# Kernel optimization log

Measured on AMD Instinct MI355X. Metric: run time of the kernel, lower is better.

Reference implementation:

```python
import jax, jax.numpy as jnp
import numpy as np

NUM_ITERATIONS = 3


def _squash_elementwise(s):
    # Faithful to original: squared_norm summed over trailing axis of size 1
    # => elementwise squash v = s^2 * s / ((1 + s^2) * sqrt(s^2))
    sq = s * s
    return sq * s / ((1.0 + sq) * jnp.sqrt(sq))


def setup_inputs() -> dict:
    key = jax.random.key(0)
    k1, k2 = jax.random.split(key)
    B, R, C, O, I = 256, 1152, 10, 16, 8
    x = jax.random.normal(k1, (B, R, I), dtype=jnp.float32)
    W = jax.random.normal(k2, (R, C, O, I), dtype=jnp.float32)
    return {"x": x, "W": W}


def reference(x, W):
    # x: (B, R, I); W: (R, C, O, I)
    R, C, O, I = W.shape
    # u_hat[b,r,c,o] = sum_i W[r,c,o,i] * x[b,r,i]   (matmul W @ x per route/capsule)
    u_hat = jnp.einsum('rcoi,bri->brco', W, x)  # (B, R, C, O)
    b_ij = jnp.zeros((R, C), dtype=x.dtype)  # batch-shared routing logits
    v = None
    for it in range(NUM_ITERATIONS):
        c_ij = jax.nn.softmax(b_ij, axis=0)  # softmax over routes (dim=1 in torch)
        s_j = jnp.einsum('rc,brco->bco', c_ij, u_hat)  # weighted sum over routes
        v = _squash_elementwise(s_j)  # (B, C, O)
        if it < NUM_ITERATIONS - 1:
            # agreement a[b,r,c] = u_hat[b,r,c,:] . v[b,c,:]
            a_ij = jnp.einsum('brco,bco->brc', u_hat, v)
            b_ij = b_ij + a_ij.mean(axis=0)  # mean over batch, batch-shared update
    return v[..., None]  # (B, C, O, 1) matches v_j.squeeze(1)
```

## Files before the change

### kernel.cpp

```cpp
#include <hip/hip_runtime.h>

static constexpr int B_ = 256;
static constexpr int R_ = 1152;
static constexpr int C_ = 10;
static constexpr int O_ = 16;
static constexpr int I_ = 8;
static constexpr int SCO = C_ * O_;
static constexpr int K_ = R_ * I_;
static constexpr int NB = 256;

typedef short bf16x8 __attribute__((ext_vector_type(8)));
typedef float f32x4  __attribute__((ext_vector_type(4)));

__device__ __forceinline__ unsigned short f2bf(float f) {
  union { float f; unsigned int u; } c; c.f = f;
  const unsigned int u = c.u;
  return (unsigned short)((u + 0x7fffu + ((u >> 16) & 1u)) >> 16);
}
__device__ __forceinline__ float bf2f(unsigned short h) {
  union { unsigned int u; float f; } c; c.u = ((unsigned int)h) << 16; return c.f;
}

__device__ __forceinline__ void gsync(unsigned int* bar, unsigned int epoch) {
  __syncthreads();
  if (threadIdx.x == 0)
    __hip_atomic_store(&bar[blockIdx.x * 16], epoch,
                       __ATOMIC_RELEASE, __HIP_MEMORY_SCOPE_AGENT);
  if (blockIdx.x == 0) {
    if (threadIdx.x < 256) {
      int guard = 0;
      while (__hip_atomic_load(&bar[threadIdx.x * 16],
                               __ATOMIC_RELAXED, __HIP_MEMORY_SCOPE_AGENT) < epoch) {
        __builtin_amdgcn_s_sleep(8);
        if (++guard > (1 << 17)) break;
      }
    }
    __syncthreads();
    if (threadIdx.x < 8)
      __hip_atomic_store(&bar[4096 + threadIdx.x * 16], epoch,
                         __ATOMIC_RELEASE, __HIP_MEMORY_SCOPE_AGENT);
  } else {
    if (threadIdx.x == 0) {
      unsigned int* g = &bar[4096 + (blockIdx.x & 7) * 16];
      int guard = 0;
      while (__hip_atomic_load(g, __ATOMIC_RELAXED,
                               __HIP_MEMORY_SCOPE_AGENT) < epoch) {
        __builtin_amdgcn_s_sleep(32);
        if (++guard > (1 << 16)) break;
      }
    }
  }
  __syncthreads();
  asm volatile("" ::: "memory");
}

__global__ __launch_bounds__(512, 1) void mega(
    const float* __restrict__ x, const float* __restrict__ W,
    float* __restrict__ out, unsigned int* __restrict__ bar,
    float* __restrict__ bvec, float* __restrict__ Z,
    unsigned short* __restrict__ xb, unsigned short* __restrict__ wraw,
    unsigned short* __restrict__ xT,
    unsigned short* __restrict__ vb0, unsigned short* __restrict__ vb1,
    unsigned short* __restrict__ wb2a, unsigned short* __restrict__ wb2b) {
  __shared__ __align__(16) unsigned char smem[82560];
  const int bx = blockIdx.x;
  const int t = threadIdx.x;
  const int lane = t & 63;
  const int w = __builtin_amdgcn_readfirstlane(t >> 6);
  const int mrow = lane & 15, quad = lane >> 4;

  if (bx == 0 && t < 32) Z[t] = 0.0f;

  if (bx < 160) {
    float* sred = (float*)smem;
    const int g = (bx & 7) * 20 + (bx >> 3);
    const int mtile = g / 10, c = g - mtile * 10;
    const int m0 = mtile * 16;
    const float* apf = x + (size_t)(m0 + mrow) * K_ + w * 1152 + quad * 8;
    const float* bpf = W + ((size_t)(w * 144 + quad) * C_ + c) * 128 + mrow * 8;
    f32x4 acc = {0.0f, 0.0f, 0.0f, 0.0f};
#pragma unroll 4
    for (int kk = 0; kk < 36; ++kk) {
      const float4 a0 = *(const float4*)(apf + kk * 32);
      const float4 a1 = *(const float4*)(apf + kk * 32 + 4);
      const float4 b0 = *(const float4*)(bpf + (size_t)kk * 5120);
      const float4 b1 = *(const float4*)(bpf + (size_t)kk * 5120 + 4);
      bf16x8 a, b;
      a[0] = (short)f2bf(a0.x); a[1] = (short)f2bf(a0.y);
      a[2] = (short)f2bf(a0.z); a[3] = (short)f2bf(a0.w);
      a[4] = (short)f2bf(a1.x); a[5] = (short)f2bf(a1.y);
      a[6] = (short)f2bf(a1.z); a[7] = (short)f2bf(a1.w);
      b[0] = (short)f2bf(b0.x); b[1] = (short)f2bf(b0.y);
      b[2] = (short)f2bf(b0.z); b[3] = (short)f2bf(b0.w);
      b[4] = (short)f2bf(b1.x); b[5] = (short)f2bf(b1.y);
      b[6] = (short)f2bf(b1.z); b[7] = (short)f2bf(b1.w);
      acc = __builtin_amdgcn_mfma_f32_16x16x32_bf16(a, b, acc, 0, 0, 0);
    }
#pragma unroll
    for (int rg = 0; rg < 4; ++rg)
      sred[w * 272 + mrow * 17 + quad * 4 + rg] = acc[rg];
    __syncthreads();
    if (t < 256) {
      const int n = t >> 4, m = t & 15;
      const int e = n * 17 + m;
      const float ss = ((sred[0 * 272 + e] + sred[1 * 272 + e]) +
                        (sred[2 * 272 + e] + sred[3 * 272 + e])) +
                       ((sred[4 * 272 + e] + sred[5 * 272 + e]) +
                        (sred[6 * 272 + e] + sred[7 * 272 + e]));
      const float s = ss * (1.0f / 1152.0f);
      const float v = s * fabsf(s) / (1.0f + s * s);
      vb0[(size_t)(c * 16 + n) * 256 + m0 + m] = f2bf(v);
    }
  } else {
    const float4* wf = (const float4*)W;
    ushort4* wr = (ushort4*)wraw;
    for (int idx = t; idx < 3840; idx += 512) {
      const int j = (bx - 160) * 3840 + idx;
      const float4 v4 = wf[j];
      ushort4 r4;
      r4.x = f2bf(v4.x); r4.y = f2bf(v4.y); r4.z = f2bf(v4.z); r4.w = f2bf(v4.w);
      wr[j] = r4;
    }
    float* sx = (float*)smem;
    for (int u = bx - 160; u < 256; u += 96) {
      const int bq = u & 3, rseg = u >> 2;
      const int rbase = rseg * 18;
      __syncthreads();
      for (int idx = t; idx < 64 * 36; idx += 512) {
        const int b = idx / 36, f4 = idx - b * 36;
        const size_t off = (size_t)(bq * 64 + b) * K_ + rbase * I_ + f4 * 4;
        const float4 val = *(const float4*)(x + off);
        ushort4 o4;
        o4.x = f2bf(val.x); o4.y = f2bf(val.y); o4.z = f2bf(val.z); o4.w = f2bf(val.w);
        *(ushort4*)(xb + off) = o4;
        const int rr = f4 >> 1, i4 = (f4 & 1) * 4;
        sx[(rr * 8 + i4 + 0) * 68 + b] = val.x;
        sx[(rr * 8 + i4 + 1) * 68 + b] = val.y;
        sx[(rr * 8 + i4 + 2) * 68 + b] = val.z;
        sx[(rr * 8 + i4 + 3) * 68 + b] = val.w;
      }
      __syncthreads();
      for (int row = w * 18; row < w * 18 + 18; ++row)
        xT[(size_t)(rseg * 144 + row) * 256 + bq * 64 + lane] = f2bf(sx[row * 68 + lane]);
    }
  }
  gsync(bar, 1);

  for (int it = 0; it < 2; ++it) {
    if (bx < 72) {
      unsigned short* svb = (unsigned short*)smem;
      float* sp = (float*)smem;
      float* sbs = (float*)(smem + 81920);
      const unsigned short* vbr = (it == 0) ? vb0 : vb1;
      unsigned short* wb2w = (it == 0) ? wb2a : wb2b;
      const int seg = (bx & 7) * 9 + (bx >> 3);
      const int r0 = seg * 16;
      const unsigned short* ap = xT + (size_t)(seg * 128 + w * 16 + mrow) * 256 + quad * 8;
      bf16x8 afr[8];
#pragma unroll
      for (int kk = 0; kk < 8; ++kk) afr[kk] = *(const bf16x8*)(ap + kk * 32);
      {
        const char* src = (const char*)vbr;
        char* dst = (char*)svb;
#pragma unroll
        for (int i = 0; i < 10; ++i) {
          const int ci = i * 512 + t;
          const int lin = ci * 16;
          const int n = ci >> 5;
          *(bf16x8*)(dst + (lin ^ ((n & 7) << 4))) = *(const bf16x8*)(src + lin);
        }
      }
      __syncthreads();
      f32x4 acc[10];
#pragma unroll
      for (int c = 0; c < 10; ++c) acc[c] = (f32x4){0.0f, 0.0f, 0.0f, 0.0f};
#pragma unroll
      for (int c = 0; c < 10; ++c) {
        const int n = c * 16 + mrow;
        const int base = n * 512 + quad * 16;
#pragma unroll
        for (int kk = 0; kk < 8; ++kk) {
          const bf16x8 b = *(const bf16x8*)((const char*)svb +
                            ((base + kk * 64) ^ ((n & 7) << 4)));
          acc[c] = __builtin_amdgcn_mfma_f32_16x16x32_bf16(afr[kk], b, acc[c], 0, 0, 0);
        }
      }
      __syncthreads();
#pragma unroll
      for (int c = 0; c < 10; ++c)
#pragma unroll
        for (int rg = 0; rg < 4; ++rg) {
          const int ml = w * 16 + quad * 4 + rg;
          sp[(c * 16 + (ml >> 3)) * 128 + mrow * 8 + (ml & 7)] = acc[c][rg];
        }
      __syncthreads();
      const int p16 = t >> 5, l32 = t & 31;
#pragma unroll
      for (int ch = 0; ch < 10; ++ch) {
        const int pair = ch * 16 + p16;
        const int rl = pair / 10, c = pair - rl * 10;
        const float4 pv = *(const float4*)&sp[(c * 16 + rl) * 128 + l32 * 4];
        const float4 wv = *(const float4*)(W + (size_t)(r0 + rl) * 1280 + c * 128 + l32 * 4);
        float prod = wv.x * pv.x + wv.y * pv.y + wv.z * pv.z + wv.w * pv.w;
        prod += __shfl_xor(prod, 1);  prod += __shfl_xor(prod, 2);
        prod += __shfl_xor(prod, 4);  prod += __shfl_xor(prod, 8);
        prod += __shfl_xor(prod, 16);
        if (l32 == 0) sbs[rl * 10 + c] = prod;
      }
      __syncthreads();
      if (t < 160) {
        const int rl = t / 10, c = t - rl * 10;
        const int r = r0 + rl;
        float b = sbs[t] * (1.0f / 256.0f);
        if (it != 0) b += bvec[r * C_ + c];
        bvec[r * C_ + c] = b;
        sbs[t] = expf(b);
      }
      __syncthreads();
      if (t < 10) {
        float z = 0.0f;
#pragma unroll
        for (int rl = 0; rl < 16; ++rl) z += sbs[rl * 10 + t];
        atomicAdd(&Z[(it + 1) * 10 + t], z);
      }
#pragma unroll
      for (int i = 0; i < 5; ++i) {
        const int base = i * 4096 + t * 8;
        const int rl = base / 1280, rem2 = base - rl * 1280;
        const int c = rem2 >> 7;
        const float e = sbs[rl * 10 + c];
        const size_t off = ((size_t)(r0 + rl) * C_ + c) * 128 + (rem2 & 127);
        const bf16x8 wv8 = *(const bf16x8*)(wraw + off);
        bf16x8 o8;
#pragma unroll
        for (int j = 0; j < 8; ++j)
          o8[j] = (short)f2bf(bf2f((unsigned short)wv8[j]) * e);
        *(bf16x8*)(wb2w + off) = o8;
      }
    }
    gsync(bar, 2 + 2 * it);

    {
      const int git = it + 1;
      if (bx < 160) {
        float* sred = (float*)smem;
        float* szed = (float*)(smem + 16384);
        const unsigned short* Bm = (git == 1) ? wb2a : wb2b;
        const int g = (bx & 7) * 20 + (bx >> 3);
        const int mtile = g / 10, c = g - mtile * 10;
        const int m0 = mtile * 16;
        const unsigned short* ap = xb + (size_t)(m0 + mrow) * K_ + w * 1152 + quad * 8;
        const unsigned short* bp = Bm + ((size_t)(w * 144 + quad) * C_ + c) * 128 + mrow * 8;
        if (t < 10) szed[t] = atomicAdd(&Z[git * 10 + t], 0.0f);
        f32x4 acc = {0.0f, 0.0f, 0.0f, 0.0f};
#pragma unroll 6
        for (int kk = 0; kk < 36; ++kk) {
          const bf16x8 a = *(const bf16x8*)(ap + kk * 32);
          const bf16x8 b = *(const bf16x8*)(bp + (size_t)kk * 5120);
          acc = __builtin_amdgcn_mfma_f32_16x16x32_bf16(a, b, acc, 0, 0, 0);
        }
#pragma unroll
        for (int rg = 0; rg < 4; ++rg)
          sred[w * 272 + mrow * 17 + quad * 4 + rg] = acc[rg];
        __syncthreads();
        if (t < 256) {
          int m, n;
          if (git == 2) { m = t >> 4; n = t & 15; } else { n = t >> 4; m = t & 15; }
          const int e = n * 17 + m;
          const float ss = ((sred[0 * 272 + e] + sred[1 * 272 + e]) +
                            (sred[2 * 272 + e] + sred[3 * 272 + e])) +
                           ((sred[4 * 272 + e] + sred[5 * 272 + e]) +
                            (sred[6 * 272 + e] + sred[7 * 272 + e]));
          const float s = ss / szed[c];
          const float v = s * fabsf(s) / (1.0f + s * s);
          if (git == 2) out[(size_t)(m0 + m) * SCO + c * 16 + n] = v;
          else          vb1[(size_t)(c * 16 + n) * 256 + m0 + m] = f2bf(v);
        }
      }
    }
    if (it == 0) gsync(bar, 3);
  }
}

extern "C" void kernel_launch(void* const* d_in, const int* in_sizes, int n_in,
                              void* d_out, int out_size, void* d_ws, size_t ws_size,
                              hipStream_t stream) {
  const float* x = (const float*)d_in[0];
  const float* W = (const float*)d_in[1];
  float* out = (float*)d_out;

  unsigned int* bar = (unsigned int*)d_ws;
  float* bvec = (float*)d_ws + 4224;
  float* Z    = bvec + R_ * C_;
  unsigned short* xb   = (unsigned short*)(Z + 32);
  unsigned short* wraw = xb + (size_t)B_ * K_;
  unsigned short* xT   = wraw + (size_t)R_ * C_ * O_ * I_;
  unsigned short* vb0  = xT + (size_t)R_ * 8 * 256;
  unsigned short* vb1  = vb0 + (size_t)160 * 256;
  unsigned short* wb2a = vb1 + (size_t)160 * 256;
  unsigned short* wb2b = wb2a + (size_t)R_ * C_ * O_ * I_;

  hipMemsetAsync(bar, 0, 16896, stream);
  mega<<<NB, 512, 0, stream>>>(x, W, out, bar, bvec, Z, xb, wraw, xT,
                               vb0, vb1, wb2a, wb2b);
}
```

Baseline: 161.5 us.

## Fold routing softmax weights into GEMM B-load instead of materializing scaled W

Removes the pre-scaled bf16 weight buffers (wb2a/wb2b). Each GEMM phase now loads the raw bf16 W and multiplies it by exp(b) weights held in LDS just before the MFMA. The preprocessing is spread evenly across all 256 blocks, so the first GEMM reads bf16 data instead of converting fp32 on the fly at the cost of one more grid barrier. The agreement phase is also split across 144 blocks of 8 routes each, with only 4 waves doing MFMA. This saves a full write and re-read of the scaled W per iteration, but adds conversion ALU work inside the GEMM inner loop.

Result: faster. 150.5 us (-6.8%).

```diff
diff --git a/kernel.cpp b/kernel.cpp
--- a/kernel.cpp
+++ b/kernel.cpp
@@ -54,14 +54,163 @@
   asm volatile("" ::: "memory");
 }
 
+__device__ __forceinline__ void gemm_phase(
+    int git, const unsigned short* __restrict__ xb,
+    const unsigned short* __restrict__ wraw, const float* __restrict__ eX,
+    float* __restrict__ Z, unsigned short* __restrict__ vbw,
+    float* __restrict__ out, unsigned char* smem,
+    int bx, int t, int w, int mrow, int quad) {
+  float* sred = (float*)smem;
+  float* szed = (float*)(smem + 16384);
+  float* e_lds = (float*)(smem + 20480);
+  const int xcd = bx & 7, j = bx >> 3;
+  const int mtile = (xcd >> 1) * 4 + j / 5;
+  const int c = (xcd & 1) * 5 + j % 5;
+  const int m0 = mtile * 16;
+  if (git > 0) {
+    for (int idx = t; idx < 1152; idx += 512) e_lds[idx] = eX[c * 1152 + idx];
+    if (t < 10) szed[t] = atomicAdd(&Z[git * 10 + t], 0.0f);
+    __syncthreads();
+  }
+  const unsigned short* ap = xb + (size_t)(m0 + mrow) * K_ + w * 1152 + quad * 8;
+  const unsigned short* bp = wraw + ((size_t)(w * 144 + quad) * C_ + c) * 128 + mrow * 8;
+  f32x4 acc = {0.0f, 0.0f, 0.0f, 0.0f};
+  if (git == 0) {
+#pragma unroll 6
+    for (int kk = 0; kk < 36; ++kk) {
+      const bf16x8 a = *(const bf16x8*)(ap + kk * 32);
+      const bf16x8 b = *(const bf16x8*)(bp + (size_t)kk * 5120);
+      acc = __builtin_amdgcn_mfma_f32_16x16x32_bf16(a, b, acc, 0, 0, 0);
+    }
+  } else {
+#pragma unroll 6
+    for (int kk = 0; kk < 36; ++kk) {
+      const bf16x8 a = *(const bf16x8*)(ap + kk * 32);
+      const bf16x8 braw = *(const bf16x8*)(bp + (size_t)kk * 5120);
+      const float ev = e_lds[w * 144 + kk * 4 + quad];
+      bf16x8 b;
+#pragma unroll
+      for (int j8 = 0; j8 < 8; ++j8)
+        b[j8] = (short)f2bf(bf2f((unsigned short)braw[j8]) * ev);
+      acc = __builtin_amdgcn_mfma_f32_16x16x32_bf16(a, b, acc, 0, 0, 0);
+    }
+  }
+#pragma unroll
+  for (int rg = 0; rg < 4; ++rg)
+    sred[w * 272 + mrow * 17 + quad * 4 + rg] = acc[rg];
+  __syncthreads();
+  if (t < 256) {
+    int m, n;
+    if (git == 2) { m = t >> 4; n = t & 15; } else { n = t >> 4; m = t & 15; }
+    const int e = n * 17 + m;
+    const float ss = ((sred[0 * 272 + e] + sred[1 * 272 + e]) +
+                      (sred[2 * 272 + e] + sred[3 * 272 + e])) +
+                     ((sred[4 * 272 + e] + sred[5 * 272 + e]) +
+                      (sred[6 * 272 + e] + sred[7 * 272 + e]));
+    const float s = (git == 0) ? ss * (1.0f / 1152.0f) : ss / szed[c];
+    const float v = s * fabsf(s) / (1.0f + s * s);
+    if (git == 2) out[(size_t)(m0 + m) * SCO + c * 16 + n] = v;
+    else          vbw[(size_t)(c * 16 + n) * 256 + m0 + m] = f2bf(v);
+  }
+}
+
+__device__ __forceinline__ void pv_phase(
+    int it, const unsigned short* __restrict__ xT,
+    const unsigned short* __restrict__ vbr, const float* __restrict__ W,
+    const unsigned short* __restrict__ wraw_unused,
+    float* __restrict__ bvec, float* __restrict__ eOut, float* __restrict__ Z,
+    unsigned char* smem, int bx, int t, int lane, int w, int mrow, int quad) {
+  unsigned short* svb = (unsigned short*)smem;
+  float* sp = (float*)smem;
+  float* sbs = (float*)(smem + 81920);
+  const int seg = (bx & 7) * 18 + (bx >> 3);
+  const int r0 = seg * 8;
+  bf16x8 afr[8];
+  if (w < 4) {
+    const unsigned short* ap = xT + (size_t)(seg * 64 + w * 16 + mrow) * 256 + quad * 8;
+#pragma unroll
+    for (int kk = 0; kk < 8; ++kk) afr[kk] = *(const bf16x8*)(ap + kk * 32);
+  }
+  {
+    const char* src = (const char*)vbr;
+    char* dst = (char*)svb;
+#pragma unroll
+    for (int i = 0; i < 10; ++i) {
+      const int ci = i * 512 + t;
+      const int lin = ci * 16;
+      const int n = ci >> 5;
+      *(bf16x8*)(dst + (lin ^ ((n & 7) << 4))) = *(const bf16x8*)(src + lin);
+    }
+  }
+  __syncthreads();
+  f32x4 acc[10];
+  if (w < 4) {
+#pragma unroll
+    for (int c = 0; c < 10; ++c) acc[c] = (f32x4){0.0f, 0.0f, 0.0f, 0.0f};
+#pragma unroll
+    for (int c = 0; c < 10; ++c) {
+      const int n = c * 16 + mrow;
+      const int base = n * 512 + quad * 16;
+#pragma unroll
+      for (int kk = 0; kk < 8; ++kk) {
+        const bf16x8 b = *(const bf16x8*)((const char*)svb +
+                          ((base + kk * 64) ^ ((n & 7) << 4)));
+        acc[c] = __builtin_amdgcn_mfma_f32_16x16x32_bf16(afr[kk], b, acc[c], 0, 0, 0);
+      }
+    }
+  }
+  __syncthreads();
+  if (w < 4) {
+#pragma unroll
+    for (int c = 0; c < 10; ++c)
+#pragma unroll
+      for (int rg = 0; rg < 4; ++rg) {
+        const int ml = w * 16 + quad * 4 + rg;
+        sp[(c * 8 + (ml >> 3)) * 128 + mrow * 8 + (ml & 7)] = acc[c][rg];
+      }
+  }
+  __syncthreads();
+  const int p16 = t >> 5, l32 = t & 31;
+#pragma unroll
+  for (int ch = 0; ch < 5; ++ch) {
+    const int pair = ch * 16 + p16;
+    const int rl = pair / 10, c = pair - rl * 10;
+    const float4 pv4 = *(const float4*)&sp[(c * 8 + rl) * 128 + l32 * 4];
+    const float4 wv = *(const float4*)(W + (size_t)(r0 + rl) * 1280 + c * 128 + l32 * 4);
+    float prod = wv.x * pv4.x + wv.y * pv4.y + wv.z * pv4.z + wv.w * pv4.w;
+    prod += __shfl_xor(prod, 1);  prod += __shfl_xor(prod, 2);
+    prod += __shfl_xor(prod, 4);  prod += __shfl_xor(prod, 8);
+    prod += __shfl_xor(prod, 16);
+    if (l32 == 0) sbs[rl * 10 + c] = prod;
+  }
+  __syncthreads();
+  if (t < 80) {
+    const int rl = t / 10, c = t - rl * 10;
+    const int r = r0 + rl;
+    float b = sbs[t] * (1.0f / 256.0f);
+    if (it != 0) b += bvec[r * C_ + c];
+    bvec[r * C_ + c] = b;
+    const float e = expf(b);
+    sbs[t] = e;
+    eOut[c * 1152 + r] = e;
+  }
+  __syncthreads();
+  if (t < 10) {
+    float z = 0.0f;
+#pragma unroll
+    for (int rl = 0; rl < 8; ++rl) z += sbs[rl * 10 + t];
+    atomicAdd(&Z[(it + 1) * 10 + t], z);
+  }
+}
+
 __global__ __launch_bounds__(512, 1) void mega(
     const float* __restrict__ x, const float* __restrict__ W,
     float* __restrict__ out, unsigned int* __restrict__ bar,
     float* __restrict__ bvec, float* __restrict__ Z,
+    float* __restrict__ eA, float* __restrict__ eB,
     unsigned short* __restrict__ xb, unsigned short* __restrict__ wraw,
     unsigned short* __restrict__ xT,
-    unsigned short* __restrict__ vb0, unsigned short* __restrict__ vb1,
-    unsigned short* __restrict__ wb2a, unsigned short* __restrict__ wb2b) {
+    unsigned short* __restrict__ vb0, unsigned short* __restrict__ vb1) {
   __shared__ __align__(16) unsigned char smem[82560];
   const int bx = blockIdx.x;
   const int t = threadIdx.x;
@@ -69,217 +218,52 @@
   const int w = __builtin_amdgcn_readfirstlane(t >> 6);
   const int mrow = lane & 15, quad = lane >> 4;
 
-  if (bx == 0 && t < 32) Z[t] = 0.0f;
-
-  if (bx < 160) {
-    float* sred = (float*)smem;
-    const int g = (bx & 7) * 20 + (bx >> 3);
-    const int mtile = g / 10, c = g - mtile * 10;
-    const int m0 = mtile * 16;
-    const float* apf = x + (size_t)(m0 + mrow) * K_ + w * 1152 + quad * 8;
-    const float* bpf = W + ((size_t)(w * 144 + quad) * C_ + c) * 128 + mrow * 8;
-    f32x4 acc = {0.0f, 0.0f, 0.0f, 0.0f};
-#pragma unroll 4
-    for (int kk = 0; kk < 36; ++kk) {
-      const float4 a0 = *(const float4*)(apf + kk * 32);
-      const float4 a1 = *(const float4*)(apf + kk * 32 + 4);
-      const float4 b0 = *(const float4*)(bpf + (size_t)kk * 5120);
-      const float4 b1 = *(const float4*)(bpf + (size_t)kk * 5120 + 4);
-      bf16x8 a, b;
-      a[0] = (short)f2bf(a0.x); a[1] = (short)f2bf(a0.y);
-      a[2] = (short)f2bf(a0.z); a[3] = (short)f2bf(a0.w);
-      a[4] = (short)f2bf(a1.x); a[5] = (short)f2bf(a1.y);
-      a[6] = (short)f2bf(a1.z); a[7] = (short)f2bf(a1.w);
-      b[0] = (short)f2bf(b0.x); b[1] = (short)f2bf(b0.y);
-      b[2] = (short)f2bf(b0.z); b[3] = (short)f2bf(b0.w);
-      b[4] = (short)f2bf(b1.x); b[5] = (short)f2bf(b1.y);
-      b[6] = (short)f2bf(b1.z); b[7] = (short)f2bf(b1.w);
-      acc = __builtin_amdgcn_mfma_f32_16x16x32_bf16(a, b, acc, 0, 0, 0);
-    }
-#pragma unroll
-    for (int rg = 0; rg < 4; ++rg)
-      sred[w * 272 + mrow * 17 + quad * 4 + rg] = acc[rg];
-    __syncthreads();
-    if (t < 256) {
-      const int n = t >> 4, m = t & 15;
-      const int e = n * 17 + m;
-      const float ss = ((sred[0 * 272 + e] + sred[1 * 272 + e]) +
-                        (sred[2 * 272 + e] + sred[3 * 272 + e])) +
-                       ((sred[4 * 272 + e] + sred[5 * 272 + e]) +
-                        (sred[6 * 272 + e] + sred[7 * 272 + e]));
-      const float s = ss * (1.0f / 1152.0f);
-      const float v = s * fabsf(s) / (1.0f + s * s);
-      vb0[(size_t)(c * 16 + n) * 256 + m0 + m] = f2bf(v);
-    }
-  } else {
+  {
     const float4* wf = (const float4*)W;
     ushort4* wr = (ushort4*)wraw;
-    for (int idx = t; idx < 3840; idx += 512) {
-      const int j = (bx - 160) * 3840 + idx;
+    for (int idx = t; idx < 1440; idx += 512) {
+      const int j = bx * 1440 + idx;
       const float4 v4 = wf[j];
       ushort4 r4;
       r4.x = f2bf(v4.x); r4.y = f2bf(v4.y); r4.z = f2bf(v4.z); r4.w = f2bf(v4.w);
       wr[j] = r4;
     }
+    if (bx == 0 && t < 32) Z[t] = 0.0f;
     float* sx = (float*)smem;
-    for (int u = bx - 160; u < 256; u += 96) {
-      const int bq = u & 3, rseg = u >> 2;
-      const int rbase = rseg * 18;
-      __syncthreads();
-      for (int idx = t; idx < 64 * 36; idx += 512) {
-        const int b = idx / 36, f4 = idx - b * 36;
-        const size_t off = (size_t)(bq * 64 + b) * K_ + rbase * I_ + f4 * 4;
-        const float4 val = *(const float4*)(x + off);
-        ushort4 o4;
-        o4.x = f2bf(val.x); o4.y = f2bf(val.y); o4.z = f2bf(val.z); o4.w = f2bf(val.w);
-        *(ushort4*)(xb + off) = o4;
-        const int rr = f4 >> 1, i4 = (f4 & 1) * 4;
-        sx[(rr * 8 + i4 + 0) * 68 + b] = val.x;
-        sx[(rr * 8 + i4 + 1) * 68 + b] = val.y;
-        sx[(rr * 8 + i4 + 2) * 68 + b] = val.z;
-        sx[(rr * 8 + i4 + 3) * 68 + b] = val.w;
-      }
-      __syncthreads();
-      for (int row = w * 18; row < w * 18 + 18; ++row)
-        xT[(size_t)(rseg * 144 + row) * 256 + bq * 64 + lane] = f2bf(sx[row * 68 + lane]);
-    }
+    const int bq = bx & 3, rseg = bx >> 2;
+    const int rbase = rseg * 18;
+    for (int idx = t; idx < 64 * 36; idx += 512) {
+      const int b = idx / 36, f4 = idx - b * 36;
+      const size_t off = (size_t)(bq * 64 + b) * K_ + rbase * I_ + f4 * 4;
+      const float4 val = *(const float4*)(x + off);
+      ushort4 o4;
+      o4.x = f2bf(val.x); o4.y = f2bf(val.y); o4.z = f2bf(val.z); o4.w = f2bf(val.w);
+      *(ushort4*)(xb + off) = o4;
+      const int rr = f4 >> 1, i4 = (f4 & 1) * 4;
+      sx[(rr * 8 + i4 + 0) * 68 + b] = val.x;
+      sx[(rr * 8 + i4 + 1) * 68 + b] = val.y;
+      sx[(rr * 8 + i4 + 2) * 68 + b] = val.z;
+      sx[(rr * 8 + i4 + 3) * 68 + b] = val.w;
+    }
+    __syncthreads();
+    for (int row = w * 18; row < w * 18 + 18; ++row)
+      xT[(size_t)(rseg * 144 + row) * 256 + bq * 64 + lane] = f2bf(sx[row * 68 + lane]);
   }
   gsync(bar, 1);
 
-  for (int it = 0; it < 2; ++it) {
-    if (bx < 72) {
-      unsigned short* svb = (unsigned short*)smem;
-      float* sp = (float*)smem;
-      float* sbs = (float*)(smem + 81920);
-      const unsigned short* vbr = (it == 0) ? vb0 : vb1;
-      unsigned short* wb2w = (it == 0) ? wb2a : wb2b;
-      const int seg = (bx & 7) * 9 + (bx >> 3);
-      const int r0 = seg * 16;
-      const unsigned short* ap = xT + (size_t)(seg * 128 + w * 16 + mrow) * 256 + quad * 8;
-      bf16x8 afr[8];
-#pragma unroll
-      for (int kk = 0; kk < 8; ++kk) afr[kk] = *(const bf16x8*)(ap + kk * 32);
-      {
-        const char* src = (const char*)vbr;
-        char* dst = (char*)svb;
-#pragma unroll
-        for (int i = 0; i < 10; ++i) {
-          const int ci = i * 512 + t;
-          const int lin = ci * 16;
-          const int n = ci >> 5;
-          *(bf16x8*)(dst + (lin ^ ((n & 7) << 4))) = *(const bf16x8*)(src + lin);
-        }
-      }
-      __syncthreads();
-      f32x4 acc[10];
-#pragma unroll
-      for (int c = 0; c < 10; ++c) acc[c] = (f32x4){0.0f, 0.0f, 0.0f, 0.0f};
-#pragma unroll
-      for (int c = 0; c < 10; ++c) {
-        const int n = c * 16 + mrow;
-        const int base = n * 512 + quad * 16;
-#pragma unroll
-        for (int kk = 0; kk < 8; ++kk) {
-          const bf16x8 b = *(const bf16x8*)((const char*)svb +
-                            ((base + kk * 64) ^ ((n & 7) << 4)));
-          acc[c] = __builtin_amdgcn_mfma_f32_16x16x32_bf16(afr[kk], b, acc[c], 0, 0, 0);
-        }
-      }
-      __syncthreads();
-#pragma unroll
-      for (int c = 0; c < 10; ++c)
-#pragma unroll
-        for (int rg = 0; rg < 4; ++rg) {
-          const int ml = w * 16 + quad * 4 + rg;
-          sp[(c * 16 + (ml >> 3)) * 128 + mrow * 8 + (ml & 7)] = acc[c][rg];
-        }
-      __syncthreads();
-      const int p16 = t >> 5, l32 = t & 31;
-#pragma unroll
-      for (int ch = 0; ch < 10; ++ch) {
-        const int pair = ch * 16 + p16;
-        const int rl = pair / 10, c = pair - rl * 10;
-        const float4 pv = *(const float4*)&sp[(c * 16 + rl) * 128 + l32 * 4];
-        const float4 wv = *(const float4*)(W + (size_t)(r0 + rl) * 1280 + c * 128 + l32 * 4);
-        float prod = wv.x * pv.x + wv.y * pv.y + wv.z * pv.z + wv.w * pv.w;
-        prod += __shfl_xor(prod, 1);  prod += __shfl_xor(prod, 2);
-        prod += __shfl_xor(prod, 4);  prod += __shfl_xor(prod, 8);
-        prod += __shfl_xor(prod, 16);
-        if (l32 == 0) sbs[rl * 10 + c] = prod;
-      }
-      __syncthreads();
-      if (t < 160) {
-        const int rl = t / 10, c = t - rl * 10;
-        const int r = r0 + rl;
-        float b = sbs[t] * (1.0f / 256.0f);
-        if (it != 0) b += bvec[r * C_ + c];
-        bvec[r * C_ + c] = b;
-        sbs[t] = expf(b);
-      }
-      __syncthreads();
-      if (t < 10) {
-        float z = 0.0f;
-#pragma unroll
-        for (int rl = 0; rl < 16; ++rl) z += sbs[rl * 10 + t];
-        atomicAdd(&Z[(it + 1) * 10 + t], z);
-      }
-#pragma unroll
-      for (int i = 0; i < 5; ++i) {
-        const int base = i * 4096 + t * 8;
-        const int rl = base / 1280, rem2 = base - rl * 1280;
-        const int c = rem2 >> 7;
-        const float e = sbs[rl * 10 + c];
-        const size_t off = ((size_t)(r0 + rl) * C_ + c) * 128 + (rem2 & 127);
-        const bf16x8 wv8 = *(const bf16x8*)(wraw + off);
-        bf16x8 o8;
-#pragma unroll
-        for (int j = 0; j < 8; ++j)
-          o8[j] = (short)f2bf(bf2f((unsigned short)wv8[j]) * e);
-        *(bf16x8*)(wb2w + off) = o8;
-      }
-    }
-    gsync(bar, 2 + 2 * it);
-
-    {
-      const int git = it + 1;
-      if (bx < 160) {
-        float* sred = (float*)smem;
-        float* szed = (float*)(smem + 16384);
-        const unsigned short* Bm = (git == 1) ? wb2a : wb2b;
-        const int g = (bx & 7) * 20 + (bx >> 3);
-        const int mtile = g / 10, c = g - mtile * 10;
-        const int m0 = mtile * 16;
-        const unsigned short* ap = xb + (size_t)(m0 + mrow) * K_ + w * 1152 + quad * 8;
-        const unsigned short* bp = Bm + ((size_t)(w * 144 + quad) * C_ + c) * 128 + mrow * 8;
-        if (t < 10) szed[t] = atomicAdd(&Z[git * 10 + t], 0.0f);
-        f32x4 acc = {0.0f, 0.0f, 0.0f, 0.0f};
-#pragma unroll 6
-        for (int kk = 0; kk < 36; ++kk) {
-          const bf16x8 a = *(const bf16x8*)(ap + kk * 32);
-          const bf16x8 b = *(const bf16x8*)(bp + (size_t)kk * 5120);
-          acc = __builtin_amdgcn_mfma_f32_16x16x32_bf16(a, b, acc, 0, 0, 0);
-        }
-#pragma unroll
-        for (int rg = 0; rg < 4; ++rg)
-          sred[w * 272 + mrow * 17 + quad * 4 + rg] = acc[rg];
-        __syncthreads();
-        if (t < 256) {
-          int m, n;
-          if (git == 2) { m = t >> 4; n = t & 15; } else { n = t >> 4; m = t & 15; }
-          const int e = n * 17 + m;
-          const float ss = ((sred[0 * 272 + e] + sred[1 * 272 + e]) +
-                            (sred[2 * 272 + e] + sred[3 * 272 + e])) +
-                           ((sred[4 * 272 + e] + sred[5 * 272 + e]) +
-                            (sred[6 * 272 + e] + sred[7 * 272 + e]));
-          const float s = ss / szed[c];
-          const float v = s * fabsf(s) / (1.0f + s * s);
-          if (git == 2) out[(size_t)(m0 + m) * SCO + c * 16 + n] = v;
-          else          vb1[(size_t)(c * 16 + n) * 256 + m0 + m] = f2bf(v);
-        }
-      }
-    }
-    if (it == 0) gsync(bar, 3);
-  }
+  if (bx < 160) gemm_phase(0, xb, wraw, nullptr, Z, vb0, out, smem, bx, t, w, mrow, quad);
+  gsync(bar, 2);
+
+  if (bx < 144) pv_phase(0, xT, vb0, W, wraw, bvec, eA, Z, smem, bx, t, lane, w, mrow, quad);
+  gsync(bar, 3);
+
+  if (bx < 160) gemm_phase(1, xb, wraw, eA, Z, vb1, out, smem, bx, t, w, mrow, quad);
+  gsync(bar, 4);
+
+  if (bx < 144) pv_phase(1, xT, vb1, W, wraw, bvec, eB, Z, smem, bx, t, lane, w, mrow, quad);
+  gsync(bar, 5);
+
+  if (bx < 160) gemm_phase(2, xb, wraw, eB, Z, nullptr, out, smem, bx, t, w, mrow, quad);
 }
 
 extern "C" void kernel_launch(void* const* d_in, const int* in_sizes, int n_in,
@@ -292,15 +276,15 @@
   unsigned int* bar = (unsigned int*)d_ws;
   float* bvec = (float*)d_ws + 4224;
   float* Z    = bvec + R_ * C_;
-  unsigned short* xb   = (unsigned short*)(Z + 32);
+  float* eA   = Z + 32;
+  float* eB   = eA + C_ * R_;
+  unsigned short* xb   = (unsigned short*)(eB + C_ * R_);
   unsigned short* wraw = xb + (size_t)B_ * K_;
   unsigned short* xT   = wraw + (size_t)R_ * C_ * O_ * I_;
   unsigned short* vb0  = xT + (size_t)R_ * 8 * 256;
   unsigned short* vb1  = vb0 + (size_t)160 * 256;
-  unsigned short* wb2a = vb1 + (size_t)160 * 256;
-  unsigned short* wb2b = wb2a + (size_t)R_ * C_ * O_ * I_;
 
   hipMemsetAsync(bar, 0, 16896, stream);
-  mega<<<NB, 512, 0, stream>>>(x, W, out, bar, bvec, Z, xb, wraw, xT,
-                               vb0, vb1, wb2a, wb2b);
-}
+  mega<<<NB, 512, 0, stream>>>(x, W, out, bar, bvec, Z, eA, eB,
+                               xb, wraw, xT, vb0, vb1);
+}
```
